# Kernel optimization log

Hardware: AMD Instinct MI355X
Metric: run time of the kernel (lower is better)

Reference implementation:

```python
import jax, jax.numpy as jnp
import numpy as np
from jax import lax

K = 7  # kernel_size
PAD = K // 2


def _feature_difference(t):
    # t: [B, C, H, W] -> normalized census-style local differences [B, K*K, H, W]
    intensity = t.mean(axis=1, keepdims=True)  # [B,1,H,W]
    # Equivalent to conv2d with the identity (eye) kernel in the torch module:
    # channel k gathers the neighbor at offset (k//K, k%K) with zero padding.
    patches = lax.conv_general_dilated_patches(
        intensity, filter_shape=(K, K), window_strides=(1, 1),
        padding=[(PAD, PAD), (PAD, PAD)])  # [B, K*K, H, W]
    local_diff = patches - intensity
    return local_diff / jnp.sqrt(0.81 + local_diff * local_diff)


def setup_inputs() -> dict:
    key = jax.random.key(0)
    kx, ky = jax.random.split(key)
    B, C, H, W = 8, 3, 320, 1024
    x = jax.random.uniform(kx, (B, C, H, W), dtype=jnp.float32)
    y = jax.random.uniform(ky, (B, C, H, W), dtype=jnp.float32)
    return {"x": x, "y": y}


def reference(x, y):
    diff_x = _feature_difference(x)
    diff_y = _feature_difference(y)
    diff_total = diff_x - lax.stop_gradient(diff_y)  # .detach() on y branch
    d2 = diff_total * diff_total
    dist = (d2 / (0.1 + d2)).mean(axis=1, keepdims=True)  # [B,1,H,W]
    b, c, h, w = x.shape
    # valid-region mask: ones in the interior, zeros in the PAD-wide border
    mask = jnp.zeros((b, 1, h, w), dtype=x.dtype)
    mask = mask.at[:, :, PAD:h - PAD, PAD:w - PAD].set(1.0)
    return (dist * mask).mean()
```

## Files before the change

### kernel.cpp

```cpp
#include <hip/hip_runtime.h>

#define PAD 3
#define HH 320
#define WW 1024
#define BB 8
#define TH 32
#define TW 64
#define HALO_H (TH + 2*PAD)
#define HALO_W (TW + 2*PAD)
#define LDS_W  72
#define RPW 8

#define NIN ((HH - 2*PAD) * (WW - 2*PAD))
#define OUT_SCALE (1.0 / (49.0 * (double)BB * (double)HH * (double)WW))
#define C0 ((float)(48.0 * (double)BB * (double)NIN * OUT_SCALE))
#define NEG_SCALE ((float)(-0.1 * OUT_SCALE))

__global__ __launch_bounds__(256) void ternary_loss_kernel(
    const float* __restrict__ x, const float* __restrict__ y,
    float* __restrict__ out)
{
    __shared__ float sIx[HALO_H][LDS_W];
    __shared__ float sIy[HALO_H][LDS_W];
    __shared__ float wave_sums[4];

    const int tile_j = blockIdx.x * TW;
    const int tile_i = blockIdx.y * TH;
    const int b      = blockIdx.z;
    const int tx  = threadIdx.x;
    const int wv  = threadIdx.y;
    const int tid = wv * 64 + tx;

    const float* xb = x + (size_t)b * 3 * HH * WW;
    const float* yb = y + (size_t)b * 3 * HH * WW;

    for (int idx = tid; idx < HALO_H * HALO_W; idx += 256) {
        int r = idx / HALO_W;
        int c = idx - r * HALO_W;
        int gi = tile_i - PAD + r;
        int gj = tile_j - PAD + c;
        float vx = 0.0f, vy = 0.0f;
        if (gi >= 0 && gi < HH && gj >= 0 && gj < WW) {
            size_t o = (size_t)gi * WW + gj;
            vx = (xb[o] + xb[(size_t)HH * WW + o] + xb[2 * (size_t)HH * WW + o]) * (1.0f / 3.0f);
            vy = (yb[o] + yb[(size_t)HH * WW + o] + yb[2 * (size_t)HH * WW + o]) * (1.0f / 3.0f);
        }
        sIx[r][c] = vx;
        sIy[r][c] = vy;
    }
    __syncthreads();

    const int gj = tile_j + tx;
    float colOK[7];
    #pragma unroll
    for (int d = 0; d < 7; ++d) {
        int nj = gj + d - 3;
        colOK[d] = (nj >= PAD && nj < WW - PAD) ? 1.0f : 0.0f;
    }

    const int li0 = wv * RPW;

    float wx[4][7], wy[4][7];
    #pragma unroll
    for (int r = 0; r < 3; ++r) {
        #pragma unroll
        for (int d = 0; d < 7; ++d) {
            wx[r][d] = sIx[li0 + 3 + r][tx + d];
            wy[r][d] = sIy[li0 + 3 + r][tx + d];
        }
    }

    float acc = 0.0f;

    #pragma unroll 1
    for (int io = 0; io < RPW / 4; ++io) {
        #pragma unroll
        for (int iu = 0; iu < 4; ++iu) {
            const int li = li0 + io * 4 + iu;
            const int gi = tile_i + li;
            const int snew = (iu + 3) & 3;
            #pragma unroll
            for (int d = 0; d < 7; ++d) {
                wx[snew][d] = sIx[li + 6][tx + d];
                wy[snew][d] = sIy[li + 6][tx + d];
            }

            float rin[4];
            #pragma unroll
            for (int di = 0; di < 4; ++di) {
                int ni = gi + di;
                rin[di] = (ni >= PAD && ni < HH - PAD) ? 1.0f : 0.0f;
            }
            const float mc = rin[0] * colOK[3];

            const float cx = wx[iu & 3][3];
            const float cy = wy[iu & 3][3];

            #pragma unroll
            for (int di = 0; di <= 3; ++di) {
                const int s = (iu + di) & 3;
                #pragma unroll
                for (int dj = -3; dj <= 3; ++dj) {
                    if (di == 0 && dj <= 0) continue;
                    float nx = wx[s][dj + 3];
                    float ny = wy[s][dj + 3];
                    float dx = nx - cx;
                    float gx = dx * __builtin_amdgcn_rsqf(fmaf(dx, dx, 0.81f));
                    float dy = ny - cy;
                    float gy = dy * __builtin_amdgcn_rsqf(fmaf(dy, dy, 0.81f));
                    float t  = gx - gy;
                    float denom = fmaf(t, t, 0.1f);
                    float r = __builtin_amdgcn_rcpf(denom);
                    float w = fmaf(rin[di], colOK[dj + 3], mc);
                    acc = fmaf(w, r, acc);
                }
            }
        }
    }

    #pragma unroll
    for (int off = 32; off > 0; off >>= 1)
        acc += __shfl_down(acc, off, 64);
    if (tx == 0) wave_sums[wv] = acc;
    __syncthreads();
    if (tid == 0) {
        float total = (wave_sums[0] + wave_sums[1] + wave_sums[2] + wave_sums[3]) * NEG_SCALE;
        if (blockIdx.x == 0 && blockIdx.y == 0 && blockIdx.z == 0)
            total += C0;
        atomicAdd(out, total);
    }
}

extern "C" void kernel_launch(void* const* d_in, const int* in_sizes, int n_in,
                              void* d_out, int out_size, void* d_ws, size_t ws_size,
                              hipStream_t stream) {
    const float* x = (const float*)d_in[0];
    const float* y = (const float*)d_in[1];
    float* out = (float*)d_out;

    hipMemsetAsync(out, 0, sizeof(float), stream);

    dim3 grid(WW / TW, HH / TH, BB);
    dim3 block(64, 4, 1);
    ternary_loss_kernel<<<grid, block, 0, stream>>>(x, y, out);
}
```

Before: 125.9 us.

## Halve tile height and add mask-free fast path for interior tiles

Tile height drops from 32 to 16 rows, so each wave handles 4 rows and the grid doubles, giving more blocks for occupancy. Tiles fully inside the valid region take a branch that skips the row and column mask arithmetic and accumulates plain reciprocals, scaled by two at the end. The register sliding window is replaced by direct LDS reads for each neighbor. The trade-off is more halo reload per output row, since halo rows are a larger share of a shorter tile, and more LDS traffic per pair in exchange for fewer FMAs and lower register pressure.

After: 130.5 us. +3.7%, slower.

```diff
diff --git a/kernel.cpp b/kernel.cpp
--- a/kernel.cpp
+++ b/kernel.cpp
@@ -4,12 +4,11 @@
 #define HH 320
 #define WW 1024
 #define BB 8
-#define TH 32
+#define TH 16
 #define TW 64
 #define HALO_H (TH + 2*PAD)
 #define HALO_W (TW + 2*PAD)
 #define LDS_W  72
-#define RPW 8
 
 #define NIN ((HH - 2*PAD) * (WW - 2*PAD))
 #define OUT_SCALE (1.0 / (49.0 * (double)BB * (double)HH * (double)WW))
@@ -50,40 +49,49 @@
     }
     __syncthreads();
 
-    const int gj = tile_j + tx;
-    float colOK[7];
-    #pragma unroll
-    for (int d = 0; d < 7; ++d) {
-        int nj = gj + d - 3;
-        colOK[d] = (nj >= PAD && nj < WW - PAD) ? 1.0f : 0.0f;
-    }
-
-    const int li0 = wv * RPW;
-
-    float wx[4][7], wy[4][7];
-    #pragma unroll
-    for (int r = 0; r < 3; ++r) {
-        #pragma unroll
-        for (int d = 0; d < 7; ++d) {
-            wx[r][d] = sIx[li0 + 3 + r][tx + d];
-            wy[r][d] = sIy[li0 + 3 + r][tx + d];
-        }
-    }
+    const bool fast = (tile_i >= 16 && tile_i <= HH - 2*TH) &&
+                      (tile_j >= TW && tile_j <= WW - 2*TW);
 
     float acc = 0.0f;
 
-    #pragma unroll 1
-    for (int io = 0; io < RPW / 4; ++io) {
+    if (fast) {
+        float accr = 0.0f;
         #pragma unroll
-        for (int iu = 0; iu < 4; ++iu) {
-            const int li = li0 + io * 4 + iu;
+        for (int k = 0; k < 4; ++k) {
+            const int li = wv * 4 + k;
+            const float cx = sIx[li + PAD][tx + PAD];
+            const float cy = sIy[li + PAD][tx + PAD];
+            #pragma unroll
+            for (int di = 0; di <= 3; ++di) {
+                #pragma unroll
+                for (int dj = -3; dj <= 3; ++dj) {
+                    if (di == 0 && dj <= 0) continue;
+                    float nx = sIx[li + PAD + di][tx + PAD + dj];
+                    float ny = sIy[li + PAD + di][tx + PAD + dj];
+                    float dx = nx - cx;
+                    float gx = dx * __builtin_amdgcn_rsqf(fmaf(dx, dx, 0.81f));
+                    float dy = ny - cy;
+                    float gy = dy * __builtin_amdgcn_rsqf(fmaf(dy, dy, 0.81f));
+                    float t  = gx - gy;
+                    accr += __builtin_amdgcn_rcpf(fmaf(t, t, 0.1f));
+                }
+            }
+        }
+        acc = 2.0f * accr;
+    } else {
+        const int gj = tile_j + tx;
+        float colOK[7];
+        #pragma unroll
+        for (int d = 0; d < 7; ++d) {
+            int nj = gj + d - 3;
+            colOK[d] = (nj >= PAD && nj < WW - PAD) ? 1.0f : 0.0f;
+        }
+        #pragma unroll
+        for (int k = 0; k < 4; ++k) {
+            const int li = wv * 4 + k;
             const int gi = tile_i + li;
-            const int snew = (iu + 3) & 3;
-            #pragma unroll
-            for (int d = 0; d < 7; ++d) {
-                wx[snew][d] = sIx[li + 6][tx + d];
-                wy[snew][d] = sIy[li + 6][tx + d];
-            }
+            const float cx = sIx[li + PAD][tx + PAD];
+            const float cy = sIy[li + PAD][tx + PAD];
 
             float rin[4];
             #pragma unroll
@@ -93,25 +101,20 @@
             }
             const float mc = rin[0] * colOK[3];
 
-            const float cx = wx[iu & 3][3];
-            const float cy = wy[iu & 3][3];
-
             #pragma unroll
             for (int di = 0; di <= 3; ++di) {
-                const int s = (iu + di) & 3;
                 #pragma unroll
                 for (int dj = -3; dj <= 3; ++dj) {
                     if (di == 0 && dj <= 0) continue;
-                    float nx = wx[s][dj + 3];
-                    float ny = wy[s][dj + 3];
+                    float nx = sIx[li + PAD + di][tx + PAD + dj];
+                    float ny = sIy[li + PAD + di][tx + PAD + dj];
                     float dx = nx - cx;
                     float gx = dx * __builtin_amdgcn_rsqf(fmaf(dx, dx, 0.81f));
                     float dy = ny - cy;
                     float gy = dy * __builtin_amdgcn_rsqf(fmaf(dy, dy, 0.81f));
                     float t  = gx - gy;
-                    float denom = fmaf(t, t, 0.1f);
-                    float r = __builtin_amdgcn_rcpf(denom);
-                    float w = fmaf(rin[di], colOK[dj + 3], mc);
+                    float r  = __builtin_amdgcn_rcpf(fmaf(t, t, 0.1f));
+                    float w  = fmaf(rin[di], colOK[dj + 3], mc);
                     acc = fmaf(w, r, acc);
                 }
             }
```

## Retile to 4x256 strips with float4 loads and 4 pixels per thread

Applied to the files above, without the earlier changes.

Replaces the 32x64 tile, where each thread walks 8 rows with a register sliding window, with a 4-row by 256-column tile. Each thread now computes 4 adjacent pixels in one row and reads rows of the intensity tile from LDS as float4 vectors. The halo covers only the 3 rows below and 4 columns on each side, matching the half-stencil symmetry, and global loads become float4. The aim is fewer LDS and global load instructions and more blocks in flight, at the cost of more redundant halo reloads from global memory per output pixel.

New measurement: 131.5 us. +4.5%, slower.

```diff
diff --git a/kernel.cpp b/kernel.cpp
--- a/kernel.cpp
+++ b/kernel.cpp
@@ -4,12 +4,11 @@
 #define HH 320
 #define WW 1024
 #define BB 8
-#define TH 32
-#define TW 64
-#define HALO_H (TH + 2*PAD)
-#define HALO_W (TW + 2*PAD)
-#define LDS_W  72
-#define RPW 8
+#define TW 256
+#define TH 4
+#define SROWS 7
+#define SCOLS 264
+#define NC4 66
 
 #define NIN ((HH - 2*PAD) * (WW - 2*PAD))
 #define OUT_SCALE (1.0 / (49.0 * (double)BB * (double)HH * (double)WW))
@@ -20,8 +19,7 @@
     const float* __restrict__ x, const float* __restrict__ y,
     float* __restrict__ out)
 {
-    __shared__ float sIx[HALO_H][LDS_W];
-    __shared__ float sIy[HALO_H][LDS_W];
+    __shared__ float sI[2][SROWS][SCOLS];
     __shared__ float wave_sums[4];
 
     const int tile_j = blockIdx.x * TW;
@@ -34,86 +32,88 @@
     const float* xb = x + (size_t)b * 3 * HH * WW;
     const float* yb = y + (size_t)b * 3 * HH * WW;
 
-    for (int idx = tid; idx < HALO_H * HALO_W; idx += 256) {
-        int r = idx / HALO_W;
-        int c = idx - r * HALO_W;
-        int gi = tile_i - PAD + r;
-        int gj = tile_j - PAD + c;
-        float vx = 0.0f, vy = 0.0f;
-        if (gi >= 0 && gi < HH && gj >= 0 && gj < WW) {
-            size_t o = (size_t)gi * WW + gj;
-            vx = (xb[o] + xb[(size_t)HH * WW + o] + xb[2 * (size_t)HH * WW + o]) * (1.0f / 3.0f);
-            vy = (yb[o] + yb[(size_t)HH * WW + o] + yb[2 * (size_t)HH * WW + o]) * (1.0f / 3.0f);
+    for (int idx = tid; idx < 2 * SROWS * NC4; idx += 256) {
+        int tsel = idx / (SROWS * NC4);
+        int rem  = idx - tsel * (SROWS * NC4);
+        int r    = rem / NC4;
+        int c4   = rem - r * NC4;
+        int gr = tile_i + r;
+        int gc = tile_j - 4 + 4 * c4;
+        float4 v = make_float4(0.f, 0.f, 0.f, 0.f);
+        if (gr < HH && gc >= 0 && gc + 3 < WW) {
+            const float* p = (tsel ? yb : xb) + (size_t)gr * WW + gc;
+            float4 a = *(const float4*)p;
+            float4 c1 = *(const float4*)(p + (size_t)HH * WW);
+            float4 c2 = *(const float4*)(p + 2 * (size_t)HH * WW);
+            v.x = (a.x + c1.x + c2.x) * (1.f / 3.f);
+            v.y = (a.y + c1.y + c2.y) * (1.f / 3.f);
+            v.z = (a.z + c1.z + c2.z) * (1.f / 3.f);
+            v.w = (a.w + c1.w + c2.w) * (1.f / 3.f);
         }
-        sIx[r][c] = vx;
-        sIy[r][c] = vy;
+        *(float4*)&sI[tsel][r][4 * c4] = v;
     }
     __syncthreads();
 
-    const int gj = tile_j + tx;
-    float colOK[7];
+    const int gi = tile_i + wv;
+    const int j0 = tile_j + 4 * tx;
+    const int lc = 4 * tx;
+
+    float colf[10];
     #pragma unroll
-    for (int d = 0; d < 7; ++d) {
-        int nj = gj + d - 3;
-        colOK[d] = (nj >= PAD && nj < WW - PAD) ? 1.0f : 0.0f;
+    for (int d = 0; d < 10; ++d) {
+        int col = j0 + d - 3;
+        colf[d] = (col >= PAD && col < WW - PAD) ? 1.f : 0.f;
+    }
+    float rowf[4];
+    #pragma unroll
+    for (int di = 0; di < 4; ++di) {
+        int rr = gi + di;
+        rowf[di] = (rr >= PAD && rr < HH - PAD) ? 1.f : 0.f;
+    }
+    float mc[4];
+    #pragma unroll
+    for (int p = 0; p < 4; ++p) mc[p] = rowf[0] * colf[p + 3];
+
+    float cx[4], cy[4];
+    {
+        float4 xa = *(const float4*)&sI[0][wv][lc + 4];
+        float4 ya = *(const float4*)&sI[1][wv][lc + 4];
+        cx[0] = xa.x; cx[1] = xa.y; cx[2] = xa.z; cx[3] = xa.w;
+        cy[0] = ya.x; cy[1] = ya.y; cy[2] = ya.z; cy[3] = ya.w;
     }
 
-    const int li0 = wv * RPW;
+    float acc = 0.f;
 
-    float wx[4][7], wy[4][7];
     #pragma unroll
-    for (int r = 0; r < 3; ++r) {
+    for (int di = 0; di <= 3; ++di) {
+        float rx[12], ry[12];
+        {
+            float4 a0 = *(const float4*)&sI[0][wv + di][lc];
+            float4 a1 = *(const float4*)&sI[0][wv + di][lc + 4];
+            float4 a2 = *(const float4*)&sI[0][wv + di][lc + 8];
+            rx[0]=a0.x; rx[1]=a0.y; rx[2]=a0.z; rx[3]=a0.w;
+            rx[4]=a1.x; rx[5]=a1.y; rx[6]=a1.z; rx[7]=a1.w;
+            rx[8]=a2.x; rx[9]=a2.y; rx[10]=a2.z; rx[11]=a2.w;
+            float4 b0 = *(const float4*)&sI[1][wv + di][lc];
+            float4 b1 = *(const float4*)&sI[1][wv + di][lc + 4];
+            float4 b2 = *(const float4*)&sI[1][wv + di][lc + 8];
+            ry[0]=b0.x; ry[1]=b0.y; ry[2]=b0.z; ry[3]=b0.w;
+            ry[4]=b1.x; ry[5]=b1.y; ry[6]=b1.z; ry[7]=b1.w;
+            ry[8]=b2.x; ry[9]=b2.y; ry[10]=b2.z; ry[11]=b2.w;
+        }
         #pragma unroll
-        for (int d = 0; d < 7; ++d) {
-            wx[r][d] = sIx[li0 + 3 + r][tx + d];
-            wy[r][d] = sIy[li0 + 3 + r][tx + d];
-        }
-    }
-
-    float acc = 0.0f;
-
-    #pragma unroll 1
-    for (int io = 0; io < RPW / 4; ++io) {
-        #pragma unroll
-        for (int iu = 0; iu < 4; ++iu) {
-            const int li = li0 + io * 4 + iu;
-            const int gi = tile_i + li;
-            const int snew = (iu + 3) & 3;
+        for (int dj = -3; dj <= 3; ++dj) {
+            if (di == 0 && dj <= 0) continue;
             #pragma unroll
-            for (int d = 0; d < 7; ++d) {
-                wx[snew][d] = sIx[li + 6][tx + d];
-                wy[snew][d] = sIy[li + 6][tx + d];
-            }
-
-            float rin[4];
-            #pragma unroll
-            for (int di = 0; di < 4; ++di) {
-                int ni = gi + di;
-                rin[di] = (ni >= PAD && ni < HH - PAD) ? 1.0f : 0.0f;
-            }
-            const float mc = rin[0] * colOK[3];
-
-            const float cx = wx[iu & 3][3];
-            const float cy = wy[iu & 3][3];
-
-            #pragma unroll
-            for (int di = 0; di <= 3; ++di) {
-                const int s = (iu + di) & 3;
-                #pragma unroll
-                for (int dj = -3; dj <= 3; ++dj) {
-                    if (di == 0 && dj <= 0) continue;
-                    float nx = wx[s][dj + 3];
-                    float ny = wy[s][dj + 3];
-                    float dx = nx - cx;
-                    float gx = dx * __builtin_amdgcn_rsqf(fmaf(dx, dx, 0.81f));
-                    float dy = ny - cy;
-                    float gy = dy * __builtin_amdgcn_rsqf(fmaf(dy, dy, 0.81f));
-                    float t  = gx - gy;
-                    float denom = fmaf(t, t, 0.1f);
-                    float r = __builtin_amdgcn_rcpf(denom);
-                    float w = fmaf(rin[di], colOK[dj + 3], mc);
-                    acc = fmaf(w, r, acc);
-                }
+            for (int p = 0; p < 4; ++p) {
+                float dx = rx[4 + p + dj] - cx[p];
+                float gx = dx * __builtin_amdgcn_rsqf(fmaf(dx, dx, 0.81f));
+                float dy = ry[4 + p + dj] - cy[p];
+                float gy = dy * __builtin_amdgcn_rsqf(fmaf(dy, dy, 0.81f));
+                float t  = gx - gy;
+                float r  = __builtin_amdgcn_rcpf(fmaf(t, t, 0.1f));
+                float w  = fmaf(rowf[di], colf[p + dj + 3], mc[p]);
+                acc = fmaf(w, r, acc);
             }
         }
     }
```
